# Optimization experiments

Measured on AMD Instinct MI355X. Metric: run time of the kernel, lower is better.

Reference implementation:

```python
import jax, jax.numpy as jnp
import numpy as np
from math import factorial

LMAX = 2
C_DIM = 128
N = 50000
# (l1, l2, l_out) 'uuu' (channel-wise, no weights) instructions, as in the module ([:3])
INSTR = [(2, 2, 0), (1, 2, 1), (1, 1, 2)]


def _f(n):
    return float(factorial(int(n)))


def _su2_cg(j1, m1, j2, m2, j3, m3):
    # Clebsch-Gordan <j1 m1 j2 m2 | j3 m3> (Racah formula), complex SU(2) basis
    if m3 != m1 + m2:
        return 0.0
    vmin = int(max(-j1 + j2 + m3, -j1 + m1, 0))
    vmax = int(min(j2 + j3 + m1, j3 - j1 + j2, j3 + m3))
    pref = ((2 * j3 + 1) * _f(j3 + j1 - j2) * _f(j3 - j1 + j2) * _f(j1 + j2 - j3) / _f(j1 + j2 + j3 + 1)
            * _f(j3 + m3) * _f(j3 - m3) / (_f(j1 - m1) * _f(j1 + m1) * _f(j2 - m2) * _f(j2 + m2))) ** 0.5
    s = 0.0
    for v in range(vmin, vmax + 1):
        s += (-1.0) ** (v + j2 + m2) / _f(v) * _f(j2 + j3 + m1 - v) * _f(j1 - m1 + v) / (
            _f(j3 - j1 + j2 - v) * _f(j3 + m3 - v) * _f(v + j1 - j2 - m3))
    return pref * s


def _q_real_to_complex(l):
    # e3nn change-of-basis from real to complex spherical harmonics
    q = np.zeros((2 * l + 1, 2 * l + 1), dtype=np.complex128)
    for m in range(-l, 0):
        q[l + m, l + abs(m)] = 1.0 / np.sqrt(2)
        q[l + m, l - abs(m)] = -1j / np.sqrt(2)
    q[l, l] = 1.0
    for m in range(1, l + 1):
        q[l + m, l + abs(m)] = (-1) ** m / np.sqrt(2)
        q[l + m, l - abs(m)] = 1j * (-1) ** m / np.sqrt(2)
    return (-1j) ** l * q


def wigner_3j(l1, l2, l3):
    # real-basis Wigner 3j, unit Frobenius norm (e3nn convention)
    Csu2 = np.zeros((2 * l1 + 1, 2 * l2 + 1, 2 * l3 + 1), dtype=np.complex128)
    for i, m1 in enumerate(range(-l1, l1 + 1)):
        for k, m2 in enumerate(range(-l2, l2 + 1)):
            for n, m3 in enumerate(range(-l3, l3 + 1)):
                Csu2[i, k, n] = _su2_cg(l1, m1, l2, m2, l3, m3)
    Q1, Q2, Q3 = _q_real_to_complex(l1), _q_real_to_complex(l2), _q_real_to_complex(l3)
    C = np.einsum('ij,kl,mn,ikn->jlm', Q1, Q2, np.conj(Q3.T), Csu2)
    assert np.abs(C.imag).max() < 1e-7
    C = C.real
    return (C / np.linalg.norm(C)).astype(np.float32)


W3J = {(l1, l2, lo): jnp.asarray(wigner_3j(l1, l2, lo)) for (l1, l2, lo) in INSTR}


def so3_linear(x, W, b):
    # per-degree block-diagonal linear; x: [N, (LMAX+1)^2, Cin], W: [LMAX+1, Cout, Cin], b: [Cout] (l=0 only)
    outs = []
    for l in range(LMAX + 1):
        y = jnp.einsum('nmc,dc->nmd', x[:, l * l:(l + 1) * (l + 1), :], W[l])
        if l == 0:
            y = y + b
        outs.append(y)
    return jnp.concatenate(outs, axis=1)


def tensor_product_uuu(x1, x2):
    # sparse CG tensor product, channel-shared ('uuu'), no path weights
    out = jnp.zeros_like(x1)
    for (l1, l2, lo) in INSTR:
        w3j = W3J[(l1, l2, lo)]
        alpha = float((2 * lo + 1) ** 0.5)  # component normalization
        blk = alpha * jnp.einsum('ijk,nic,njc->nkc', w3j,
                                 x1[:, l1 * l1:(l1 + 1) ** 2, :],
                                 x2[:, l2 * l2:(l2 + 1) ** 2, :])
        out = out.at[:, lo * lo:(lo + 1) ** 2, :].add(blk)
    return out


def setup_inputs() -> dict:
    key = jax.random.key(0)
    ks = jax.random.split(key, 7)
    scale = 1.0 / np.sqrt(C_DIM)
    m_dim = (LMAX + 1) ** 2  # 9
    return {
        'irreps_x': jax.random.normal(ks[0], (N, m_dim, C_DIM), jnp.float32),
        'W_left': jax.random.normal(ks[1], (LMAX + 1, C_DIM, C_DIM), jnp.float32) * scale,
        'b_left': jax.random.normal(ks[2], (C_DIM,), jnp.float32) * scale,
        'W_right': jax.random.normal(ks[3], (LMAX + 1, C_DIM, C_DIM), jnp.float32) * scale,
        'b_right': jax.random.normal(ks[4], (C_DIM,), jnp.float32) * scale,
        'W_final': jax.random.normal(ks[5], (LMAX + 1, C_DIM, C_DIM), jnp.float32) * scale,
        'b_final': jax.random.normal(ks[6], (C_DIM,), jnp.float32) * scale,
    }


def reference(irreps_x, W_left, b_left, W_right, b_right, W_final, b_final):
    xl = so3_linear(irreps_x, W_left, b_left)
    xr = so3_linear(irreps_x, W_right, b_right)
    out = tensor_product_uuu(xl, xr)
    return so3_linear(out, W_final, b_final)  # [N, 9, C]
```

## Files before the change

kernel.cpp:

```cpp
#include <hip/hip_runtime.h>
#include <cmath>
#include <complex>

typedef unsigned short u16;
typedef unsigned int u32;
typedef __bf16 bf16x8 __attribute__((ext_vector_type(8)));
typedef __bf16 bf16x2 __attribute__((ext_vector_type(2)));
typedef float f32x4 __attribute__((ext_vector_type(4)));
typedef float f32x2 __attribute__((ext_vector_type(2)));

#define CD 128
#define TILE_N 8
#define XS 136
#define CS 66

#define SMEM_TOTAL (72 * XS + 2 * 128 * CS)

struct TPW { float w220[25]; float w121[45]; float w112[45]; };

__device__ __forceinline__ u32 pk2(float a, float b) {
  bf16x2 h;
  h.x = (__bf16)a;
  h.y = (__bf16)b;
  return __builtin_bit_cast(u32, h);
}
__device__ __forceinline__ f32x2 unpk(u32 v) {
  f32x2 r;
  r.x = __uint_as_float(v << 16);
  r.y = __uint_as_float(v & 0xffff0000u);
  return r;
}

__device__ __forceinline__ void ldw4(uint4* dst, const u16* base) {
#pragma unroll
  for (int kk = 0; kk < 4; ++kk)
    dst[kk] = *(const uint4*)(base + kk * 32);
}

__device__ __forceinline__ f32x4 mf(const uint4& a, const uint4& b, f32x4 c) {
  return __builtin_amdgcn_mfma_f32_16x16x32_bf16(
      __builtin_bit_cast(bf16x8, a), __builtin_bit_cast(bf16x8, b), c, 0, 0, 0);
}

__device__ __forceinline__ void stA(u16* d, const f32x4& a) {
  u32* p = (u32*)d;
  p[0] = pk2(a[0], a[1]);
  p[1] = pk2(a[2], a[3]);
}

__global__ void cvt_weights_kernel(const float* __restrict__ Wl,
                                   const float* __restrict__ Wr,
                                   const float* __restrict__ Wf,
                                   u16* __restrict__ ws) {
  int idx = (blockIdx.x * 256 + threadIdx.x) * 8;
  const float* src; int off;
  if (idx < 49152)      { src = Wl; off = idx; }
  else if (idx < 98304) { src = Wr; off = idx - 49152; }
  else                  { src = Wf; off = idx - 98304; }
  float4 a = *(const float4*)(src + off);
  float4 b = *(const float4*)(src + off + 4);
  uint4 v;
  v.x = pk2(a.x, a.y);
  v.y = pk2(a.z, a.w);
  v.z = pk2(b.x, b.y);
  v.w = pk2(b.z, b.w);
  *(uint4*)(ws + idx) = v;
}

__global__ __launch_bounds__(256, 3)
void fused_kernel(const float* __restrict__ x, const u16* __restrict__ ws,
                  const float* __restrict__ bfin, float* __restrict__ out,
                  int N, TPW tw) {
  __shared__ __align__(16) u16 smem[SMEM_TOTAL];
  u16* bufX = smem;
  u16* sTP  = smem;
  u16* sL   = smem + 72 * XS;
  u16* sR   = sL + 128 * CS;

  const int tid  = threadIdx.x;
  const int n0   = blockIdx.x * TILE_N;
  const int w    = tid >> 6;
  const int lane = tid & 63;
  const int q    = lane >> 4;
  const int lr   = lane & 15;

  const int mat = w >> 1;
  const int wl  = w & 1;
  u16* dstA = mat ? sR : sL;
  const u16* wsA = ws + mat * 3 * 16384;
  const u16* wsf = ws + 6 * 16384;

  const int dc0 = w * 16 + lr;
  const int dc1 = dc0 + 64;
  const float bias0 = bfin[dc0];
  const float bias1 = bfin[dc1];

#pragma unroll
  for (int it = 0; it < 4; ++it) {
    int e = (it * 256 + tid) * 8;
    int r = e >> 7;
    int c = e & 127;
    int n = n0 + (r & 7);
    if (n >= N) n = N - 1;
    int grow = (n * 9 + 1 + (r >> 3)) * CD + c;
    float4 a = *(const float4*)(x + grow);
    float4 b = *(const float4*)(x + grow + 4);
    uint4 v;
    v.x = pk2(a.x, a.y);
    v.y = pk2(a.z, a.w);
    v.z = pk2(b.x, b.y);
    v.w = pk2(b.z, b.w);
    *(uint4*)(bufX + r * XS + c) = v;
  }

  const int colb = wl * 64 + lr;
  uint4 wf0[4], wf1[4], wf2[4], wf3[4];
  ldw4(wf0, wsA + 16384 + (colb     ) * CD + q * 8);
  ldw4(wf1, wsA + 16384 + (colb + 16) * CD + q * 8);
  ldw4(wf2, wsA + 16384 + (colb + 32) * CD + q * 8);
  ldw4(wf3, wsA + 16384 + (colb + 48) * CD + q * 8);
  __syncthreads();

#pragma unroll
  for (int rt = 0; rt < 2; ++rt) {
    const int gbase = rt * 16;
    int ga = gbase + lr; if (ga > 23) ga = 23;
    uint4 av[4];
    ldw4(av, bufX + ga * XS + q * 8);
    f32x4 a0 = {0.f,0.f,0.f,0.f}, a1 = {0.f,0.f,0.f,0.f};
    f32x4 a2 = {0.f,0.f,0.f,0.f}, a3 = {0.f,0.f,0.f,0.f};
#pragma unroll
    for (int kk = 0; kk < 4; ++kk) {
      a0 = mf(av[kk], wf0[kk], a0);
      a1 = mf(av[kk], wf1[kk], a1);
      a2 = mf(av[kk], wf2[kk], a2);
      a3 = mf(av[kk], wf3[kk], a3);
    }
    int g0 = gbase + q * 4;
    if (g0 < 24) {
      stA(dstA + (colb     ) * CS + g0, a0);
      stA(dstA + (colb + 16) * CS + g0, a1);
      stA(dstA + (colb + 32) * CS + g0, a2);
      stA(dstA + (colb + 48) * CS + g0, a3);
    }
  }
  ldw4(wf0, wsA + 2 * 16384 + (colb     ) * CD + q * 8);
  ldw4(wf1, wsA + 2 * 16384 + (colb + 16) * CD + q * 8);
  ldw4(wf2, wsA + 2 * 16384 + (colb + 32) * CD + q * 8);
  ldw4(wf3, wsA + 2 * 16384 + (colb + 48) * CD + q * 8);
#pragma unroll
  for (int rt = 0; rt < 3; ++rt) {
    const int gbase = rt * 16;
    int ga = gbase + lr; if (ga > 39) ga = 39;
    uint4 av[4];
    ldw4(av, bufX + (24 + ga) * XS + q * 8);
    f32x4 a0 = {0.f,0.f,0.f,0.f}, a1 = {0.f,0.f,0.f,0.f};
    f32x4 a2 = {0.f,0.f,0.f,0.f}, a3 = {0.f,0.f,0.f,0.f};
#pragma unroll
    for (int kk = 0; kk < 4; ++kk) {
      a0 = mf(av[kk], wf0[kk], a0);
      a1 = mf(av[kk], wf1[kk], a1);
      a2 = mf(av[kk], wf2[kk], a2);
      a3 = mf(av[kk], wf3[kk], a3);
    }
    int g0 = gbase + q * 4;
    if (g0 < 40) {
      stA(dstA + (colb     ) * CS + 24 + g0, a0);
      stA(dstA + (colb + 16) * CS + 24 + g0, a1);
      stA(dstA + (colb + 32) * CS + 24 + g0, a2);
      stA(dstA + (colb + 48) * CS + 24 + g0, a3);
    }
  }
  __syncthreads();

#pragma unroll
  for (int iter = 0; iter < 2; ++iter) {
    int id = iter * 256 + tid;
    int ch = id & 127;
    int n  = (id >> 7) * 2;
    const u16* pL = sL + ch * CS + n;
    const u16* pR = sR + ch * CS + n;
    f32x2 xl1[3], xr1[3], xl2[5], xr2[5];
#pragma unroll
    for (int i = 0; i < 3; ++i) {
      xl1[i] = unpk(*(const u32*)(pL + i * 8));
      xr1[i] = unpk(*(const u32*)(pR + i * 8));
    }
#pragma unroll
    for (int j = 0; j < 5; ++j) {
      xl2[j] = unpk(*(const u32*)(pL + 24 + j * 8));
      xr2[j] = unpk(*(const u32*)(pR + 24 + j * 8));
    }
    f32x2 o0 = {0.f, 0.f};
#pragma unroll
    for (int i = 0; i < 5; ++i) {
      f32x2 t = {0.f, 0.f};
#pragma unroll
      for (int j = 0; j < 5; ++j) t += tw.w220[i * 5 + j] * xr2[j];
      o0 += xl2[i] * t;
    }
    f32x2 o1[3] = {{0.f,0.f},{0.f,0.f},{0.f,0.f}};
#pragma unroll
    for (int i = 0; i < 3; ++i)
#pragma unroll
      for (int j = 0; j < 5; ++j) {
        f32x2 pr = xl1[i] * xr2[j];
#pragma unroll
        for (int k = 0; k < 3; ++k) o1[k] += tw.w121[(i * 5 + j) * 3 + k] * pr;
      }
    f32x2 o2[5] = {{0.f,0.f},{0.f,0.f},{0.f,0.f},{0.f,0.f},{0.f,0.f}};
#pragma unroll
    for (int i = 0; i < 3; ++i)
#pragma unroll
      for (int j = 0; j < 3; ++j) {
        f32x2 pr = xl1[i] * xr1[j];
#pragma unroll
        for (int k = 0; k < 5; ++k) o2[k] += tw.w112[(i * 3 + j) * 5 + k] * pr;
      }
    u16* pT = sTP + n * XS + ch;
    u32 v0 = pk2(o0.x, o0.y);
    pT[0]  = (u16)v0;
    pT[XS] = (u16)(v0 >> 16);
#pragma unroll
    for (int k = 0; k < 3; ++k) {
      u32 v = pk2(o1[k].x, o1[k].y);
      u16* b = pT + (1 + k) * 8 * XS;
      b[0]  = (u16)v;
      b[XS] = (u16)(v >> 16);
    }
#pragma unroll
    for (int k = 0; k < 5; ++k) {
      u32 v = pk2(o2[k].x, o2[k].y);
      u16* b = pT + (4 + k) * 8 * XS;
      b[0]  = (u16)v;
      b[XS] = (u16)(v >> 16);
    }
  }

  uint4 bc0[4], bc1[4];
  ldw4(bc0, wsf + dc0 * CD + q * 8);
  ldw4(bc1, wsf + dc1 * CD + q * 8);
  __syncthreads();

#pragma unroll
  for (int l = 0; l < 3; ++l) {
    if (l > 0) {
      ldw4(bc0, wsf + l * 16384 + dc0 * CD + q * 8);
      ldw4(bc1, wsf + l * 16384 + dc1 * CD + q * 8);
    }
    const int rows   = (l == 0) ? 8 : (l == 1 ? 24 : 40);
    const int soff   = (l == 0) ? 0 : (l == 1 ? 8 : 32);
    const int ntl    = (l == 0) ? 1 : (l == 1 ? 2 : 3);
#pragma unroll
    for (int t = 0; t < 3; ++t) {
      if (t >= ntl) continue;
      int ga = t * 16 + lr; if (ga > rows - 1) ga = rows - 1;
      uint4 av[4];
      ldw4(av, sTP + (soff + ga) * XS + q * 8);
      f32x4 a0 = {0.f, 0.f, 0.f, 0.f};
      f32x4 a1 = {0.f, 0.f, 0.f, 0.f};
#pragma unroll
      for (int kk = 0; kk < 4; ++kk) {
        a0 = mf(av[kk], bc0[kk], a0);
        a1 = mf(av[kk], bc1[kk], a1);
      }
#pragma unroll
      for (int reg = 0; reg < 4; ++reg) {
        int gg = t * 16 + q * 4 + reg;
        if (gg < rows) {
          int m = l * l + (gg >> 3);
          int n = n0 + (gg & 7);
          if (n < N) {
            float v0 = a0[reg], v1 = a1[reg];
            if (l == 0) { v0 += bias0; v1 += bias1; }
            out[(n * 9 + m) * CD + dc0] = v0;
            out[(n * 9 + m) * CD + dc1] = v1;
          }
        }
      }
    }
  }
}

typedef std::complex<double> cd;

static double factd(int n) { double r = 1.0; for (int i = 2; i <= n; ++i) r *= i; return r; }

static double su2_cg(int j1, int m1, int j2, int m2, int j3, int m3) {
  if (m3 != m1 + m2) return 0.0;
  int vmin = -j1 + j2 + m3; if (-j1 + m1 > vmin) vmin = -j1 + m1; if (0 > vmin) vmin = 0;
  int vmax = j2 + j3 + m1; if (j3 - j1 + j2 < vmax) vmax = j3 - j1 + j2; if (j3 + m3 < vmax) vmax = j3 + m3;
  double pref = std::sqrt((2.0 * j3 + 1.0) * factd(j3 + j1 - j2) * factd(j3 - j1 + j2)
                          * factd(j1 + j2 - j3) / factd(j1 + j2 + j3 + 1)
                          * factd(j3 + m3) * factd(j3 - m3)
                          / (factd(j1 - m1) * factd(j1 + m1) * factd(j2 - m2) * factd(j2 + m2)));
  double s = 0.0;
  for (int v = vmin; v <= vmax; ++v) {
    double sgn = ((v + j2 + m2) & 1) ? -1.0 : 1.0;
    s += sgn / factd(v) * factd(j2 + j3 + m1 - v) * factd(j1 - m1 + v)
         / (factd(j3 - j1 + j2 - v) * factd(j3 + m3 - v) * factd(v + j1 - j2 - m3));
  }
  return pref * s;
}

static void qmat(int l, cd q[5][5]) {
  for (int a = 0; a < 5; ++a) for (int b = 0; b < 5; ++b) q[a][b] = 0.0;
  const double is2 = 1.0 / std::sqrt(2.0);
  for (int m = -l; m < 0; ++m) {
    q[l + m][l - m] = is2;
    q[l + m][l + m] = cd(0.0, -is2);
  }
  q[l][l] = 1.0;
  for (int m = 1; m <= l; ++m) {
    double s = (m & 1) ? -1.0 : 1.0;
    q[l + m][l + m] = s * is2;
    q[l + m][l - m] = cd(0.0, s * is2);
  }
  cd f(1.0, 0.0);
  for (int i = 0; i < l; ++i) f *= cd(0.0, -1.0);
  for (int a = 0; a < 5; ++a) for (int b = 0; b < 5; ++b) q[a][b] *= f;
}

static void wigner3j(int l1, int l2, int l3, double* C) {
  int d1 = 2 * l1 + 1, d2 = 2 * l2 + 1, d3 = 2 * l3 + 1;
  cd Q1[5][5], Q2[5][5], Q3[5][5];
  qmat(l1, Q1); qmat(l2, Q2); qmat(l3, Q3);
  cd Csu2[5][5][5];
  for (int i = 0; i < d1; ++i)
    for (int k = 0; k < d2; ++k)
      for (int n = 0; n < d3; ++n)
        Csu2[i][k][n] = su2_cg(l1, i - l1, l2, k - l2, l3, n - l3);
  double norm = 0.0;
  for (int j = 0; j < d1; ++j)
    for (int lx = 0; lx < d2; ++lx)
      for (int m = 0; m < d3; ++m) {
        cd acc(0.0, 0.0);
        for (int i = 0; i < d1; ++i)
          for (int k = 0; k < d2; ++k)
            for (int n = 0; n < d3; ++n)
              acc += Q1[i][j] * Q2[k][lx] * std::conj(Q3[n][m]) * Csu2[i][k][n];
        C[(j * d2 + lx) * d3 + m] = acc.real();
        norm += acc.real() * acc.real();
      }
  norm = std::sqrt(norm);
  for (int t = 0; t < d1 * d2 * d3; ++t) C[t] /= norm;
}

extern "C" void kernel_launch(void* const* d_in, const int* in_sizes, int n_in,
                              void* d_out, int out_size, void* d_ws, size_t ws_size,
                              hipStream_t stream) {
  const float* x    = (const float*)d_in[0];
  const float* Wl   = (const float*)d_in[1];
  const float* Wr   = (const float*)d_in[3];
  const float* Wf   = (const float*)d_in[5];
  const float* bfin = (const float*)d_in[6];
  float* out = (float*)d_out;
  const int N = in_sizes[0] / (9 * CD);

  TPW tw;
  double c220[25], c121[45], c112[45];
  wigner3j(2, 2, 0, c220);
  wigner3j(1, 2, 1, c121);
  wigner3j(1, 1, 2, c112);
  const double a1 = std::sqrt(3.0), a2 = std::sqrt(5.0);
  for (int i = 0; i < 25; ++i) tw.w220[i] = (float)c220[i];
  for (int i = 0; i < 45; ++i) tw.w121[i] = (float)(a1 * c121[i]);
  for (int i = 0; i < 45; ++i) tw.w112[i] = (float)(a2 * c112[i]);

  u16* ws = (u16*)d_ws;
  cvt_weights_kernel<<<72, 256, 0, stream>>>(Wl, Wr, Wf, ws);
  int grid = (N + TILE_N - 1) / TILE_N;
  fused_kernel<<<grid, 256, 0, stream>>>(x, ws, bfin, out, N, tw);
}
```

Baseline: 493.9 us.

## Process multiple tiles per block with register prefetch of next tile input

Each block now loops over four node tiles instead of one. It prefetches the next tile's input into registers while computing the l=2 projection of the current tile. Block barriers are replaced by a barrier that waits only on LDS counters, so outstanding global loads can cross it. This aims to hide global load latency and amortize block startup, at the cost of extra registers and a smaller grid with possible tail imbalance.

```diff
diff --git a/kernel.cpp b/kernel.cpp
--- a/kernel.cpp
+++ b/kernel.cpp
@@ -11,12 +11,17 @@
 
 #define CD 128
 #define TILE_N 8
+#define KTILES 4
 #define XS 136
 #define CS 66
 
 #define SMEM_TOTAL (72 * XS + 2 * 128 * CS)
 
 struct TPW { float w220[25]; float w121[45]; float w112[45]; };
+
+__device__ __forceinline__ void softbar() {
+  asm volatile("s_waitcnt lgkmcnt(0)\n\ts_barrier" ::: "memory");
+}
 
 __device__ __forceinline__ u32 pk2(float a, float b) {
   bf16x2 h;
@@ -78,7 +83,6 @@
   u16* sR   = sL + 128 * CS;
 
   const int tid  = threadIdx.x;
-  const int n0   = blockIdx.x * TILE_N;
   const int w    = tid >> 6;
   const int lane = tid & 63;
   const int q    = lane >> 4;
@@ -95,186 +99,212 @@
   const float bias0 = bfin[dc0];
   const float bias1 = bfin[dc1];
 
-#pragma unroll
-  for (int it = 0; it < 4; ++it) {
-    int e = (it * 256 + tid) * 8;
-    int r = e >> 7;
-    int c = e & 127;
-    int n = n0 + (r & 7);
-    if (n >= N) n = N - 1;
-    int grow = (n * 9 + 1 + (r >> 3)) * CD + c;
-    float4 a = *(const float4*)(x + grow);
-    float4 b = *(const float4*)(x + grow + 4);
-    uint4 v;
-    v.x = pk2(a.x, a.y);
-    v.y = pk2(a.z, a.w);
-    v.z = pk2(b.x, b.y);
-    v.w = pk2(b.z, b.w);
-    *(uint4*)(bufX + r * XS + c) = v;
-  }
-
-  const int colb = wl * 64 + lr;
-  uint4 wf0[4], wf1[4], wf2[4], wf3[4];
-  ldw4(wf0, wsA + 16384 + (colb     ) * CD + q * 8);
-  ldw4(wf1, wsA + 16384 + (colb + 16) * CD + q * 8);
-  ldw4(wf2, wsA + 16384 + (colb + 32) * CD + q * 8);
-  ldw4(wf3, wsA + 16384 + (colb + 48) * CD + q * 8);
-  __syncthreads();
-
-#pragma unroll
-  for (int rt = 0; rt < 2; ++rt) {
-    const int gbase = rt * 16;
-    int ga = gbase + lr; if (ga > 23) ga = 23;
-    uint4 av[4];
-    ldw4(av, bufX + ga * XS + q * 8);
-    f32x4 a0 = {0.f,0.f,0.f,0.f}, a1 = {0.f,0.f,0.f,0.f};
-    f32x4 a2 = {0.f,0.f,0.f,0.f}, a3 = {0.f,0.f,0.f,0.f};
-#pragma unroll
-    for (int kk = 0; kk < 4; ++kk) {
-      a0 = mf(av[kk], wf0[kk], a0);
-      a1 = mf(av[kk], wf1[kk], a1);
-      a2 = mf(av[kk], wf2[kk], a2);
-      a3 = mf(av[kk], wf3[kk], a3);
-    }
-    int g0 = gbase + q * 4;
-    if (g0 < 24) {
-      stA(dstA + (colb     ) * CS + g0, a0);
-      stA(dstA + (colb + 16) * CS + g0, a1);
-      stA(dstA + (colb + 32) * CS + g0, a2);
-      stA(dstA + (colb + 48) * CS + g0, a3);
-    }
-  }
-  ldw4(wf0, wsA + 2 * 16384 + (colb     ) * CD + q * 8);
-  ldw4(wf1, wsA + 2 * 16384 + (colb + 16) * CD + q * 8);
-  ldw4(wf2, wsA + 2 * 16384 + (colb + 32) * CD + q * 8);
-  ldw4(wf3, wsA + 2 * 16384 + (colb + 48) * CD + q * 8);
-#pragma unroll
-  for (int rt = 0; rt < 3; ++rt) {
-    const int gbase = rt * 16;
-    int ga = gbase + lr; if (ga > 39) ga = 39;
-    uint4 av[4];
-    ldw4(av, bufX + (24 + ga) * XS + q * 8);
-    f32x4 a0 = {0.f,0.f,0.f,0.f}, a1 = {0.f,0.f,0.f,0.f};
-    f32x4 a2 = {0.f,0.f,0.f,0.f}, a3 = {0.f,0.f,0.f,0.f};
-#pragma unroll
-    for (int kk = 0; kk < 4; ++kk) {
-      a0 = mf(av[kk], wf0[kk], a0);
-      a1 = mf(av[kk], wf1[kk], a1);
-      a2 = mf(av[kk], wf2[kk], a2);
-      a3 = mf(av[kk], wf3[kk], a3);
-    }
-    int g0 = gbase + q * 4;
-    if (g0 < 40) {
-      stA(dstA + (colb     ) * CS + 24 + g0, a0);
-      stA(dstA + (colb + 16) * CS + 24 + g0, a1);
-      stA(dstA + (colb + 32) * CS + 24 + g0, a2);
-      stA(dstA + (colb + 48) * CS + 24 + g0, a3);
-    }
-  }
-  __syncthreads();
-
-#pragma unroll
-  for (int iter = 0; iter < 2; ++iter) {
-    int id = iter * 256 + tid;
-    int ch = id & 127;
-    int n  = (id >> 7) * 2;
-    const u16* pL = sL + ch * CS + n;
-    const u16* pR = sR + ch * CS + n;
-    f32x2 xl1[3], xr1[3], xl2[5], xr2[5];
-#pragma unroll
-    for (int i = 0; i < 3; ++i) {
-      xl1[i] = unpk(*(const u32*)(pL + i * 8));
-      xr1[i] = unpk(*(const u32*)(pR + i * 8));
-    }
-#pragma unroll
-    for (int j = 0; j < 5; ++j) {
-      xl2[j] = unpk(*(const u32*)(pL + 24 + j * 8));
-      xr2[j] = unpk(*(const u32*)(pR + 24 + j * 8));
-    }
-    f32x2 o0 = {0.f, 0.f};
-#pragma unroll
-    for (int i = 0; i < 5; ++i) {
-      f32x2 t = {0.f, 0.f};
-#pragma unroll
-      for (int j = 0; j < 5; ++j) t += tw.w220[i * 5 + j] * xr2[j];
-      o0 += xl2[i] * t;
-    }
-    f32x2 o1[3] = {{0.f,0.f},{0.f,0.f},{0.f,0.f}};
-#pragma unroll
-    for (int i = 0; i < 3; ++i)
+  const int ntiles = (N + TILE_N - 1) / TILE_N;
+  const int tile0  = blockIdx.x * KTILES;
+  const int colb   = wl * 64 + lr;
+
+  auto LOADX = [&](int tile, float4* xv) {
+    const int nb = tile * TILE_N;
+#pragma unroll
+    for (int it = 0; it < 4; ++it) {
+      const int e = (it * 256 + tid) * 8;
+      const int r = e >> 7;
+      const int c = e & 127;
+      int n = nb + (r & 7);
+      if (n >= N) n = N - 1;
+      const int grow = (n * 9 + 1 + (r >> 3)) * CD + c;
+      xv[2 * it]     = *(const float4*)(x + grow);
+      xv[2 * it + 1] = *(const float4*)(x + grow + 4);
+    }
+  };
+
+  float4 xv[8];
+  LOADX(tile0, xv);
+
+#pragma unroll 1
+  for (int t = 0; t < KTILES; ++t) {
+    const int tile = tile0 + t;
+    if (tile >= ntiles) break;
+    const int n0 = tile * TILE_N;
+
+    if (t > 0) softbar();
+
+#pragma unroll
+    for (int it = 0; it < 4; ++it) {
+      const int e = (it * 256 + tid) * 8;
+      const int r = e >> 7;
+      const int c = e & 127;
+      uint4 v;
+      v.x = pk2(xv[2 * it].x,     xv[2 * it].y);
+      v.y = pk2(xv[2 * it].z,     xv[2 * it].w);
+      v.z = pk2(xv[2 * it + 1].x, xv[2 * it + 1].y);
+      v.w = pk2(xv[2 * it + 1].z, xv[2 * it + 1].w);
+      *(uint4*)(bufX + r * XS + c) = v;
+    }
+
+    uint4 wf0[4], wf1[4], wf2[4], wf3[4];
+    ldw4(wf0, wsA + 16384 + (colb     ) * CD + q * 8);
+    ldw4(wf1, wsA + 16384 + (colb + 16) * CD + q * 8);
+    ldw4(wf2, wsA + 16384 + (colb + 32) * CD + q * 8);
+    ldw4(wf3, wsA + 16384 + (colb + 48) * CD + q * 8);
+    softbar();
+
+#pragma unroll
+    for (int rt = 0; rt < 2; ++rt) {
+      const int gbase = rt * 16;
+      int ga = gbase + lr; if (ga > 23) ga = 23;
+      uint4 av[4];
+      ldw4(av, bufX + ga * XS + q * 8);
+      f32x4 a0 = {0.f,0.f,0.f,0.f}, a1 = {0.f,0.f,0.f,0.f};
+      f32x4 a2 = {0.f,0.f,0.f,0.f}, a3 = {0.f,0.f,0.f,0.f};
+#pragma unroll
+      for (int kk = 0; kk < 4; ++kk) {
+        a0 = mf(av[kk], wf0[kk], a0);
+        a1 = mf(av[kk], wf1[kk], a1);
+        a2 = mf(av[kk], wf2[kk], a2);
+        a3 = mf(av[kk], wf3[kk], a3);
+      }
+      int g0 = gbase + q * 4;
+      if (g0 < 24) {
+        stA(dstA + (colb     ) * CS + g0, a0);
+        stA(dstA + (colb + 16) * CS + g0, a1);
+        stA(dstA + (colb + 32) * CS + g0, a2);
+        stA(dstA + (colb + 48) * CS + g0, a3);
+      }
+    }
+    ldw4(wf0, wsA + 2 * 16384 + (colb     ) * CD + q * 8);
+    ldw4(wf1, wsA + 2 * 16384 + (colb + 16) * CD + q * 8);
+    ldw4(wf2, wsA + 2 * 16384 + (colb + 32) * CD + q * 8);
+    ldw4(wf3, wsA + 2 * 16384 + (colb + 48) * CD + q * 8);
+    if (t + 1 < KTILES && tile + 1 < ntiles) LOADX(tile + 1, xv);
+#pragma unroll
+    for (int rt = 0; rt < 3; ++rt) {
+      const int gbase = rt * 16;
+      int ga = gbase + lr; if (ga > 39) ga = 39;
+      uint4 av[4];
+      ldw4(av, bufX + (24 + ga) * XS + q * 8);
+      f32x4 a0 = {0.f,0.f,0.f,0.f}, a1 = {0.f,0.f,0.f,0.f};
+      f32x4 a2 = {0.f,0.f,0.f,0.f}, a3 = {0.f,0.f,0.f,0.f};
+#pragma unroll
+      for (int kk = 0; kk < 4; ++kk) {
+        a0 = mf(av[kk], wf0[kk], a0);
+        a1 = mf(av[kk], wf1[kk], a1);
+        a2 = mf(av[kk], wf2[kk], a2);
+        a3 = mf(av[kk], wf3[kk], a3);
+      }
+      int g0 = gbase + q * 4;
+      if (g0 < 40) {
+        stA(dstA + (colb     ) * CS + 24 + g0, a0);
+        stA(dstA + (colb + 16) * CS + 24 + g0, a1);
+        stA(dstA + (colb + 32) * CS + 24 + g0, a2);
+        stA(dstA + (colb + 48) * CS + 24 + g0, a3);
+      }
+    }
+    softbar();
+
+#pragma unroll
+    for (int iter = 0; iter < 2; ++iter) {
+      int id = iter * 256 + tid;
+      int ch = id & 127;
+      int n  = (id >> 7) * 2;
+      const u16* pL = sL + ch * CS + n;
+      const u16* pR = sR + ch * CS + n;
+      f32x2 xl1[3], xr1[3], xl2[5], xr2[5];
+#pragma unroll
+      for (int i = 0; i < 3; ++i) {
+        xl1[i] = unpk(*(const u32*)(pL + i * 8));
+        xr1[i] = unpk(*(const u32*)(pR + i * 8));
+      }
 #pragma unroll
       for (int j = 0; j < 5; ++j) {
-        f32x2 pr = xl1[i] * xr2[j];
-#pragma unroll
-        for (int k = 0; k < 3; ++k) o1[k] += tw.w121[(i * 5 + j) * 3 + k] * pr;
-      }
-    f32x2 o2[5] = {{0.f,0.f},{0.f,0.f},{0.f,0.f},{0.f,0.f},{0.f,0.f}};
-#pragma unroll
-    for (int i = 0; i < 3; ++i)
-#pragma unroll
-      for (int j = 0; j < 3; ++j) {
-        f32x2 pr = xl1[i] * xr1[j];
-#pragma unroll
-        for (int k = 0; k < 5; ++k) o2[k] += tw.w112[(i * 3 + j) * 5 + k] * pr;
-      }
-    u16* pT = sTP + n * XS + ch;
-    u32 v0 = pk2(o0.x, o0.y);
-    pT[0]  = (u16)v0;
-    pT[XS] = (u16)(v0 >> 16);
-#pragma unroll
-    for (int k = 0; k < 3; ++k) {
-      u32 v = pk2(o1[k].x, o1[k].y);
-      u16* b = pT + (1 + k) * 8 * XS;
-      b[0]  = (u16)v;
-      b[XS] = (u16)(v >> 16);
-    }
-#pragma unroll
-    for (int k = 0; k < 5; ++k) {
-      u32 v = pk2(o2[k].x, o2[k].y);
-      u16* b = pT + (4 + k) * 8 * XS;
-      b[0]  = (u16)v;
-      b[XS] = (u16)(v >> 16);
-    }
-  }
-
-  uint4 bc0[4], bc1[4];
-  ldw4(bc0, wsf + dc0 * CD + q * 8);
-  ldw4(bc1, wsf + dc1 * CD + q * 8);
-  __syncthreads();
-
-#pragma unroll
-  for (int l = 0; l < 3; ++l) {
-    if (l > 0) {
-      ldw4(bc0, wsf + l * 16384 + dc0 * CD + q * 8);
-      ldw4(bc1, wsf + l * 16384 + dc1 * CD + q * 8);
-    }
-    const int rows   = (l == 0) ? 8 : (l == 1 ? 24 : 40);
-    const int soff   = (l == 0) ? 0 : (l == 1 ? 8 : 32);
-    const int ntl    = (l == 0) ? 1 : (l == 1 ? 2 : 3);
-#pragma unroll
-    for (int t = 0; t < 3; ++t) {
-      if (t >= ntl) continue;
-      int ga = t * 16 + lr; if (ga > rows - 1) ga = rows - 1;
-      uint4 av[4];
-      ldw4(av, sTP + (soff + ga) * XS + q * 8);
-      f32x4 a0 = {0.f, 0.f, 0.f, 0.f};
-      f32x4 a1 = {0.f, 0.f, 0.f, 0.f};
-#pragma unroll
-      for (int kk = 0; kk < 4; ++kk) {
-        a0 = mf(av[kk], bc0[kk], a0);
-        a1 = mf(av[kk], bc1[kk], a1);
-      }
-#pragma unroll
-      for (int reg = 0; reg < 4; ++reg) {
-        int gg = t * 16 + q * 4 + reg;
-        if (gg < rows) {
-          int m = l * l + (gg >> 3);
-          int n = n0 + (gg & 7);
-          if (n < N) {
-            float v0 = a0[reg], v1 = a1[reg];
-            if (l == 0) { v0 += bias0; v1 += bias1; }
-            out[(n * 9 + m) * CD + dc0] = v0;
-            out[(n * 9 + m) * CD + dc1] = v1;
+        xl2[j] = unpk(*(const u32*)(pL + 24 + j * 8));
+        xr2[j] = unpk(*(const u32*)(pR + 24 + j * 8));
+      }
+      f32x2 o0 = {0.f, 0.f};
+#pragma unroll
+      for (int i = 0; i < 5; ++i) {
+        f32x2 s = {0.f, 0.f};
+#pragma unroll
+        for (int j = 0; j < 5; ++j) s += tw.w220[i * 5 + j] * xr2[j];
+        o0 += xl2[i] * s;
+      }
+      f32x2 o1[3] = {{0.f,0.f},{0.f,0.f},{0.f,0.f}};
+#pragma unroll
+      for (int i = 0; i < 3; ++i)
+#pragma unroll
+        for (int j = 0; j < 5; ++j) {
+          f32x2 pr = xl1[i] * xr2[j];
+#pragma unroll
+          for (int k = 0; k < 3; ++k) o1[k] += tw.w121[(i * 5 + j) * 3 + k] * pr;
+        }
+      f32x2 o2[5] = {{0.f,0.f},{0.f,0.f},{0.f,0.f},{0.f,0.f},{0.f,0.f}};
+#pragma unroll
+      for (int i = 0; i < 3; ++i)
+#pragma unroll
+        for (int j = 0; j < 3; ++j) {
+          f32x2 pr = xl1[i] * xr1[j];
+#pragma unroll
+          for (int k = 0; k < 5; ++k) o2[k] += tw.w112[(i * 3 + j) * 5 + k] * pr;
+        }
+      u16* pT = sTP + n * XS + ch;
+      u32 v0 = pk2(o0.x, o0.y);
+      pT[0]  = (u16)v0;
+      pT[XS] = (u16)(v0 >> 16);
+#pragma unroll
+      for (int k = 0; k < 3; ++k) {
+        u32 v = pk2(o1[k].x, o1[k].y);
+        u16* b = pT + (1 + k) * 8 * XS;
+        b[0]  = (u16)v;
+        b[XS] = (u16)(v >> 16);
+      }
+#pragma unroll
+      for (int k = 0; k < 5; ++k) {
+        u32 v = pk2(o2[k].x, o2[k].y);
+        u16* b = pT + (4 + k) * 8 * XS;
+        b[0]  = (u16)v;
+        b[XS] = (u16)(v >> 16);
+      }
+    }
+
+    uint4 bc0[4], bc1[4];
+    ldw4(bc0, wsf + dc0 * CD + q * 8);
+    ldw4(bc1, wsf + dc1 * CD + q * 8);
+    softbar();
+
+#pragma unroll
+    for (int l = 0; l < 3; ++l) {
+      if (l > 0) {
+        ldw4(bc0, wsf + l * 16384 + dc0 * CD + q * 8);
+        ldw4(bc1, wsf + l * 16384 + dc1 * CD + q * 8);
+      }
+      const int rows = (l == 0) ? 8 : (l == 1 ? 24 : 40);
+      const int soff = (l == 0) ? 0 : (l == 1 ? 8 : 32);
+      const int ntl  = (l == 0) ? 1 : (l == 1 ? 2 : 3);
+#pragma unroll
+      for (int tt = 0; tt < 3; ++tt) {
+        if (tt >= ntl) continue;
+        int ga = tt * 16 + lr; if (ga > rows - 1) ga = rows - 1;
+        uint4 av[4];
+        ldw4(av, sTP + (soff + ga) * XS + q * 8);
+        f32x4 a0 = {0.f, 0.f, 0.f, 0.f};
+        f32x4 a1 = {0.f, 0.f, 0.f, 0.f};
+#pragma unroll
+        for (int kk = 0; kk < 4; ++kk) {
+          a0 = mf(av[kk], bc0[kk], a0);
+          a1 = mf(av[kk], bc1[kk], a1);
+        }
+#pragma unroll
+        for (int reg = 0; reg < 4; ++reg) {
+          int gg = tt * 16 + q * 4 + reg;
+          if (gg < rows) {
+            int m = l * l + (gg >> 3);
+            int n = n0 + (gg & 7);
+            if (n < N) {
+              float v0 = a0[reg], v1 = a1[reg];
+              if (l == 0) { v0 += bias0; v1 += bias1; }
+              out[(n * 9 + m) * CD + dc0] = v0;
+              out[(n * 9 + m) * CD + dc1] = v1;
+            }
           }
         }
       }
@@ -369,6 +399,7 @@
 
   u16* ws = (u16*)d_ws;
   cvt_weights_kernel<<<72, 256, 0, stream>>>(Wl, Wr, Wf, ws);
-  int grid = (N + TILE_N - 1) / TILE_N;
+  int ntiles = (N + TILE_N - 1) / TILE_N;
+  int grid = (ntiles + KTILES - 1) / KTILES;
   fused_kernel<<<grid, 256, 0, stream>>>(x, ws, bfin, out, N, tw);
 }
```

Measured after the change: 590.2 us. +19.5%, slower.
